# Kernel optimization log

Measured on AMD Instinct MI355X. Metric: run time of the kernel, lower is better.

The kernel has to match this reference:

```python
import jax, jax.numpy as jnp
import numpy as np

SQ, SK, D, DV = 4096, 4096, 1024, 1024


def setup_inputs() -> dict:
    key = jax.random.key(0)
    kq, kk, kv = jax.random.split(key, 3)
    Q = jax.random.normal(kq, (SQ, D), dtype=jnp.float32)
    K = jax.random.normal(kk, (SK, D), dtype=jnp.float32)
    V = jax.random.normal(kv, (SK, DV), dtype=jnp.float32)
    return {"Q": Q, "K": K, "V": V}


def reference(Q, K, V):
    # scores: [Sq, Sk]; scaled by K.shape[0] (NOT sqrt(d_k)) per original module
    scores = jnp.matmul(Q, K.T) / K.shape[0]
    # softmax over dim=0 (the QUERY axis), matching torch F.softmax(..., dim=0)
    attn = jax.nn.softmax(scores, axis=0)
    return jnp.matmul(attn, V)  # [Sq, Dv]
```

## Files before the change

kernel.cpp:

```cpp
#include <hip/hip_runtime.h>
#include <hip/hip_bf16.h>
#include <stdint.h>

#define SQ_  4096
#define SK_  4096
#define D_   1024
#define DV_  1024

typedef __attribute__((ext_vector_type(4))) float  f32x4;
typedef __attribute__((ext_vector_type(4))) int    i32x4;
typedef __attribute__((ext_vector_type(8))) int    i32x8;

__device__ __forceinline__ unsigned f2fp4(float x) {
  unsigned sgn = (__float_as_uint(x) >> 28) & 0x8u;
  float y = fabsf(x);
  unsigned c;
  if (y < 1.75f)      c = (unsigned)(int)rintf(y + y);
  else if (y < 2.5f)  c = 4u;
  else if (y < 3.5f)  c = 5u;
  else if (y < 5.0f)  c = 6u;
  else                c = 7u;
  return sgn | c;
}

__device__ __forceinline__ void gload_lds16(const void* gp, void* lp) {
  auto g1 = reinterpret_cast<__attribute__((address_space(1))) uint32_t*>(
      reinterpret_cast<uintptr_t>(gp));
  auto l3 = reinterpret_cast<__attribute__((address_space(3))) uint32_t*>(
      reinterpret_cast<uintptr_t>(lp));
  __builtin_amdgcn_global_load_lds(g1, l3, 16, 0, 0);
}

__global__ void conv4_dual_kernel(const float* __restrict__ Q,
                                  const float* __restrict__ Km,
                                  unsigned int* __restrict__ Q4,
                                  unsigned int* __restrict__ K4) {
  const int half = SQ_ * D_ / 8;
  int i = blockIdx.x * blockDim.x + threadIdx.x;
  const float* in = (i < half) ? Q : Km;
  unsigned int* out = (i < half) ? Q4 : K4;
  int ii = (i < half) ? i : i - half;
  const float4* p = reinterpret_cast<const float4*>(in) + (size_t)ii * 2;
  float4 v0 = p[0], v1 = p[1];
  unsigned w = 0;
  w |= f2fp4(2.0f * v0.x);
  w |= f2fp4(2.0f * v0.y) << 4;
  w |= f2fp4(2.0f * v0.z) << 8;
  w |= f2fp4(2.0f * v0.w) << 12;
  w |= f2fp4(2.0f * v1.x) << 16;
  w |= f2fp4(2.0f * v1.y) << 20;
  w |= f2fp4(2.0f * v1.z) << 24;
  w |= f2fp4(2.0f * v1.w) << 28;
  out[ii] = w;
}

__global__ void transv_cs_kernel(const float* __restrict__ V,
                                 const float* __restrict__ part,
                                 unsigned char* __restrict__ V4t,
                                 float* __restrict__ cs_part) {
  __shared__ float tile[64][65];
  __shared__ float linv[64];
  __shared__ float red[4][64];
  __shared__ float csred[4][64];
  int j0 = blockIdx.x * 64;
  int d0 = blockIdx.y * 64;
  int t  = threadIdx.x;
  int tr = t >> 6;
  int tc = t & 63;
  {
    float s = 0.f;
    #pragma unroll
    for (int k = 0; k < 8; ++k)
      s += part[(size_t)(tr * 8 + k) * SK_ + j0 + tc];
    red[tr][tc] = s;
  }
  #pragma unroll
  for (int rr = 0; rr < 16; ++rr) {
    int j = rr * 4 + tr;
    tile[j][tc] = V[(size_t)(j0 + j) * DV_ + d0 + tc];
  }
  __syncthreads();
  if (t < 64)
    linv[t] = 1.0f / (4096.0f + red[0][t] + red[1][t] + red[2][t] + red[3][t]);
  __syncthreads();
  float sc = 8192.0f * linv[tc];
  #pragma unroll
  for (int rr = 0; rr < 16; ++rr) {
    int d = rr * 4 + tr;
    unsigned c = f2fp4(tile[tc][d] * sc);
    unsigned pc = __shfl_xor(c, 1, 64);
    if ((tc & 1) == 0)
      V4t[(size_t)(d0 + d) * (SK_ / 2) + (j0 + tc) / 2] =
          (unsigned char)(c | (pc << 4));
  }
  float s = 0.f;
  #pragma unroll
  for (int jj = 0; jj < 16; ++jj) {
    int j = tr * 16 + jj;
    s += tile[j][tc] * linv[j];
  }
  csred[tr][tc] = s;
  __syncthreads();
  if (tr == 0)
    cs_part[(size_t)blockIdx.x * DV_ + d0 + tc] =
        csred[0][tc] + csred[1][tc] + csred[2][tc] + csred[3][tc];
}

template <int FM, int FN, int MODE>
__global__ __launch_bounds__(256, 2)
void gemm4_kernel(const unsigned char* __restrict__ A,
                  const unsigned char* __restrict__ B,
                  void* __restrict__ Cout,
                  const float* __restrict__ cs_part,
                  float* __restrict__ part,
                  int N, int Kelem, float scale) {
  constexpr int BM = FM * 32;
  constexpr int BN = FN * 32;
  __shared__ __align__(16) unsigned char As[2][BM * 64];
  __shared__ __align__(16) unsigned char Bs[2][BN * 64];
  __shared__ float csL[BN];

  const int t    = threadIdx.x;
  const int lane = t & 63;
  const int wave = t >> 6;
  const int wr   = wave >> 1, wc = wave & 1;
  const int lr   = lane & 15;
  const int lk   = lane >> 4;
  const int m0 = blockIdx.y * BM;
  const int n0 = blockIdx.x * BN;
  const int KB = Kelem / 2;

  if constexpr (MODE == 1) {
    if (t < BN) {
      float s = 0.f;
      #pragma unroll
      for (int p = 0; p < 64; ++p) s += cs_part[(size_t)p * DV_ + n0 + t];
      csL[t] = s;
    }
  }

  f32x4 acc[FM][FN] = {};

  auto stage = [&](int buf, int k0B) {
    #pragma unroll
    for (int it = 0; it < FM / 2; ++it) {
      int s = it * 256 + t;
      int row = s >> 2, p = s & 3;
      int pl = p ^ ((row >> 1) & 3);
      gload_lds16(A + (size_t)(m0 + row) * KB + k0B + pl * 16,
                  &As[buf][s * 16]);
    }
    #pragma unroll
    for (int it = 0; it < FN / 2; ++it) {
      int s = it * 256 + t;
      int row = s >> 2, p = s & 3;
      int pl = p ^ ((row >> 1) & 3);
      gload_lds16(B + (size_t)(n0 + row) * KB + k0B + pl * 16,
                  &Bs[buf][s * 16]);
    }
  };

  stage(0, 0);
  __syncthreads();
  int cur = 0;
  for (int k0B = 0; k0B < KB; k0B += 64) {
    if (k0B + 64 < KB) stage(cur ^ 1, k0B + 64);

    i32x8 af[FM], bfr[FN];
    #pragma unroll
    for (int m = 0; m < FM; ++m) {
      int r = wr * (FM * 16) + m * 16 + lr;
      int sl = lk ^ ((r >> 1) & 3);
      i32x4 lo = *reinterpret_cast<const i32x4*>(&As[cur][r * 64 + sl * 16]);
      af[m][0] = lo[0]; af[m][1] = lo[1]; af[m][2] = lo[2]; af[m][3] = lo[3];
      af[m][4] = 0; af[m][5] = 0; af[m][6] = 0; af[m][7] = 0;
    }
    #pragma unroll
    for (int n = 0; n < FN; ++n) {
      int r = wc * (FN * 16) + n * 16 + lr;
      int sl = lk ^ ((r >> 1) & 3);
      i32x4 lo = *reinterpret_cast<const i32x4*>(&Bs[cur][r * 64 + sl * 16]);
      bfr[n][0] = lo[0]; bfr[n][1] = lo[1]; bfr[n][2] = lo[2]; bfr[n][3] = lo[3];
      bfr[n][4] = 0; bfr[n][5] = 0; bfr[n][6] = 0; bfr[n][7] = 0;
    }
    #pragma unroll
    for (int m = 0; m < FM; ++m)
      #pragma unroll
      for (int n = 0; n < FN; ++n)
        acc[m][n] = __builtin_amdgcn_mfma_scale_f32_16x16x128_f8f6f4(
            af[m], bfr[n], acc[m][n], 4, 4, 0, 127, 0, 127);

    __syncthreads();
    cur ^= 1;
  }

  const int orow0 = m0 + wr * (FM * 16) + lk * 4;
  const int ocol0 = n0 + wc * (FN * 16) + lr;
  if constexpr (MODE == 0) {
    unsigned char* E4 = (unsigned char*)Cout;
    float csum[FN];
    #pragma unroll
    for (int n = 0; n < FN; ++n) csum[n] = 0.f;
    #pragma unroll
    for (int m = 0; m < FM; ++m)
      #pragma unroll
      for (int n = 0; n < FN; ++n)
        #pragma unroll
        for (int r = 0; r < 4; ++r) {
          float s = acc[m][n][r] * scale;
          float e = s + 0.5f * s * s + (1.0f / 6.0f) * s * s * s;
          csum[n] += e;
          unsigned c = f2fp4(e * 128.0f);
          unsigned pc = __shfl_xor(c, 1, 64);
          if ((lr & 1) == 0)
            E4[(size_t)(orow0 + m * 16 + r) * (N / 2) +
               ((ocol0 + n * 16) >> 1)] = (unsigned char)(c | (pc << 4));
        }
    #pragma unroll
    for (int n = 0; n < FN; ++n) {
      csum[n] += __shfl_xor(csum[n], 16, 64);
      csum[n] += __shfl_xor(csum[n], 32, 64);
    }
    float* scr = (float*)&As[0][0];
    if (wr == 0 && lane < 16) {
      #pragma unroll
      for (int n = 0; n < FN; ++n)
        scr[wc * (FN * 16) + n * 16 + lane] = csum[n];
    }
    __syncthreads();
    if (wr == 1 && lane < 16) {
      #pragma unroll
      for (int n = 0; n < FN; ++n)
        part[(size_t)blockIdx.y * SK_ + n0 + wc * (FN * 16) + n * 16 + lane] =
            scr[wc * (FN * 16) + n * 16 + lane] + csum[n];
    }
  } else {
    float* O = (float*)Cout;
    #pragma unroll
    for (int m = 0; m < FM; ++m)
      #pragma unroll
      for (int n = 0; n < FN; ++n) {
        float cs = csL[wc * (FN * 16) + n * 16 + lr];
        #pragma unroll
        for (int r = 0; r < 4; ++r)
          O[(size_t)(orow0 + m * 16 + r) * N + (ocol0 + n * 16)] =
              cs + acc[m][n][r] * (1.0f / 1048576.0f);
      }
  }
}

extern "C" void kernel_launch(void* const* d_in, const int* in_sizes, int n_in,
                              void* d_out, int out_size, void* d_ws,
                              size_t ws_size, hipStream_t stream) {
  const float* Q = (const float*)d_in[0];
  const float* K = (const float*)d_in[1];
  const float* V = (const float*)d_in[2];

  char* ws = (char*)d_ws;
  unsigned char* Q4   = (unsigned char*)(ws);
  unsigned char* K4   = (unsigned char*)(ws + ((size_t)2 << 20));
  unsigned char* e4   = (unsigned char*)(ws + ((size_t)4 << 20));
  unsigned char* V4t  = (unsigned char*)(ws + ((size_t)12 << 20));
  float*         part = (float*)(ws + ((size_t)14 << 20));
  float*         csp  = (float*)(ws + ((size_t)15 << 20));

  conv4_dual_kernel<<<(SQ_ + SK_) * D_ / 8 / 256, 256, 0, stream>>>(
      Q, K, (unsigned*)Q4, (unsigned*)K4);

  gemm4_kernel<4, 4, 0><<<dim3(SK_ / 128, SQ_ / 128), 256, 0, stream>>>(
      Q4, K4, (void*)e4, nullptr, part, SK_, D_, 1.0f / 16384.0f);

  transv_cs_kernel<<<dim3(SK_ / 64, DV_ / 64), 256, 0, stream>>>(
      V, part, V4t, csp);

  gemm4_kernel<2, 4, 1><<<dim3(DV_ / 128, SQ_ / 64), 256, 0, stream>>>(
      e4, V4t, d_out, csp, nullptr, DV_, SK_, 1.0f);

  (void)in_sizes; (void)n_in; (void)out_size; (void)ws_size;
}
```

Measured before the change: 66.82 us.

## Restructure FP4 GEMM pipeline with explicit vmcnt waits and XCD-aware block swizzle

Turns the GEMM main loop into a two-ahead prefetch. Both LDS buffers are staged up front, and each iteration waits on a partial vmcnt and uses raw s_barrier instead of a full __syncthreads. It also remaps workgroup IDs so consecutive tiles land on the same XCD chunk for better L2 locality, and raises wave priority around the MFMA block. K is made a compile-time template parameter. The hand-counted vmcnt values depend on the per-stage load count, and issuing the next stage into the current buffer right after the LDS reads relies on the extra barrier being correct.

Result: no change. 66.91 us (+0.1%).

```diff
diff --git a/kernel.cpp b/kernel.cpp
--- a/kernel.cpp
+++ b/kernel.cpp
@@ -106,16 +106,19 @@
         csred[0][tc] + csred[1][tc] + csred[2][tc] + csred[3][tc];
 }
 
-template <int FM, int FN, int MODE>
+template <int FM, int FN, int MODE, int KELEM>
 __global__ __launch_bounds__(256, 2)
 void gemm4_kernel(const unsigned char* __restrict__ A,
                   const unsigned char* __restrict__ B,
                   void* __restrict__ Cout,
                   const float* __restrict__ cs_part,
                   float* __restrict__ part,
-                  int N, int Kelem, float scale) {
+                  int N, float scale) {
   constexpr int BM = FM * 32;
   constexpr int BN = FN * 32;
+  constexpr int KB = KELEM / 2;
+  constexpr int NT = KB / 64;
+  constexpr int LOADS = FM / 2 + FN / 2;
   __shared__ __align__(16) unsigned char As[2][BM * 64];
   __shared__ __align__(16) unsigned char Bs[2][BN * 64];
   __shared__ float csL[BN];
@@ -126,9 +129,15 @@
   const int wr   = wave >> 1, wc = wave & 1;
   const int lr   = lane & 15;
   const int lk   = lane >> 4;
-  const int m0 = blockIdx.y * BM;
-  const int n0 = blockIdx.x * BN;
-  const int KB = Kelem / 2;
+
+  const int nwg  = gridDim.x * gridDim.y;
+  const int orig = blockIdx.y * gridDim.x + blockIdx.x;
+  const int cpx  = nwg >> 3;
+  const int swz  = (orig & 7) * cpx + (orig >> 3);
+  const int bx   = swz % gridDim.x;
+  const int by   = swz / gridDim.x;
+  const int m0   = by * BM;
+  const int n0   = bx * BN;
 
   if constexpr (MODE == 1) {
     if (t < BN) {
@@ -161,10 +170,17 @@
   };
 
   stage(0, 0);
-  __syncthreads();
-  int cur = 0;
-  for (int k0B = 0; k0B < KB; k0B += 64) {
-    if (k0B + 64 < KB) stage(cur ^ 1, k0B + 64);
+  stage(1, 64);
+  #pragma unroll 2
+  for (int tt = 0; tt < NT; ++tt) {
+    const int cur = tt & 1;
+    if (tt + 1 < NT) {
+      if constexpr (LOADS == 4) asm volatile("s_waitcnt vmcnt(4)" ::: "memory");
+      else                      asm volatile("s_waitcnt vmcnt(3)" ::: "memory");
+    } else {
+      asm volatile("s_waitcnt vmcnt(0)" ::: "memory");
+    }
+    __builtin_amdgcn_s_barrier();
 
     i32x8 af[FM], bfr[FN];
     #pragma unroll
@@ -183,15 +199,19 @@
       bfr[n][0] = lo[0]; bfr[n][1] = lo[1]; bfr[n][2] = lo[2]; bfr[n][3] = lo[3];
       bfr[n][4] = 0; bfr[n][5] = 0; bfr[n][6] = 0; bfr[n][7] = 0;
     }
+    asm volatile("s_waitcnt lgkmcnt(0)" ::: "memory");
+    __builtin_amdgcn_sched_barrier(0);
+    __builtin_amdgcn_s_barrier();
+    if (tt + 2 < NT) stage(cur, (tt + 2) * 64);
+
+    __builtin_amdgcn_s_setprio(1);
     #pragma unroll
     for (int m = 0; m < FM; ++m)
       #pragma unroll
       for (int n = 0; n < FN; ++n)
         acc[m][n] = __builtin_amdgcn_mfma_scale_f32_16x16x128_f8f6f4(
             af[m], bfr[n], acc[m][n], 4, 4, 0, 127, 0, 127);
-
-    __syncthreads();
-    cur ^= 1;
+    __builtin_amdgcn_s_setprio(0);
   }
 
   const int orow0 = m0 + wr * (FM * 16) + lk * 4;
@@ -231,7 +251,7 @@
     if (wr == 1 && lane < 16) {
       #pragma unroll
       for (int n = 0; n < FN; ++n)
-        part[(size_t)blockIdx.y * SK_ + n0 + wc * (FN * 16) + n * 16 + lane] =
+        part[(size_t)by * SK_ + n0 + wc * (FN * 16) + n * 16 + lane] =
             scr[wc * (FN * 16) + n * 16 + lane] + csum[n];
     }
   } else {
@@ -267,14 +287,14 @@
   conv4_dual_kernel<<<(SQ_ + SK_) * D_ / 8 / 256, 256, 0, stream>>>(
       Q, K, (unsigned*)Q4, (unsigned*)K4);
 
-  gemm4_kernel<4, 4, 0><<<dim3(SK_ / 128, SQ_ / 128), 256, 0, stream>>>(
-      Q4, K4, (void*)e4, nullptr, part, SK_, D_, 1.0f / 16384.0f);
+  gemm4_kernel<4, 4, 0, D_><<<dim3(SK_ / 128, SQ_ / 128), 256, 0, stream>>>(
+      Q4, K4, (void*)e4, nullptr, part, SK_, 1.0f / 16384.0f);
 
   transv_cs_kernel<<<dim3(SK_ / 64, DV_ / 64), 256, 0, stream>>>(
       V, part, V4t, csp);
 
-  gemm4_kernel<2, 4, 1><<<dim3(DV_ / 128, SQ_ / 64), 256, 0, stream>>>(
-      e4, V4t, d_out, csp, nullptr, DV_, SK_, 1.0f);
+  gemm4_kernel<2, 4, 1, SK_><<<dim3(DV_ / 128, SQ_ / 64), 256, 0, stream>>>(
+      e4, V4t, d_out, csp, nullptr, DV_, 1.0f);
 
   (void)in_sizes; (void)n_in; (void)out_size; (void)ws_size;
 }
```
